# Optimization experiments

Hardware: AMD Instinct MI355X
Metric: run time of the kernel (lower is better)

## Reference

```python
import jax, jax.numpy as jnp
import numpy as np

N_NODES = 100_000
N_EDGES_RAND = 800_000
N_GRAPHS = 2048
IN_FEATS = 74        # CanonicalAtomFeaturizer size
HEADS = 4            # dgllife GAT default num_heads
OUT_FEATS = 32       # dgllife GAT default hidden_feats=[32,32]
PRED_DIM = 128
NEG_SLOPE = 0.2      # dgllife default alpha


def setup_inputs() -> dict:
    key = jax.random.key(0)
    ks = jax.random.split(key, 16)
    feats = jax.random.normal(ks[0], (N_NODES, IN_FEATS), jnp.float32)
    src_r = jax.random.randint(ks[1], (N_EDGES_RAND,), 0, N_NODES, dtype=jnp.int32)
    dst_r = jax.random.randint(ks[2], (N_EDGES_RAND,), 0, N_NODES, dtype=jnp.int32)
    loops = jnp.arange(N_NODES, dtype=jnp.int32)  # self-loops -> no zero in-degree
    src = jnp.concatenate([src_r, loops])
    dst = jnp.concatenate([dst_r, loops])
    # sorted, every graph non-empty, ~49 nodes per molecule
    graph_ids = ((jnp.arange(N_NODES, dtype=jnp.int64) * N_GRAPHS) // N_NODES).astype(jnp.int32)

    def lin(k, i, o):
        return (jax.random.normal(k, (i, o), jnp.float32) / np.sqrt(i)).astype(jnp.float32)

    HF = HEADS * OUT_FEATS
    return {
        'feats': feats, 'src': src, 'dst': dst, 'graph_ids': graph_ids,
        'fc1_w': lin(ks[3], IN_FEATS, HF),
        'attn_l1': jax.random.normal(ks[4], (HEADS, OUT_FEATS), jnp.float32) * 0.1,
        'attn_r1': jax.random.normal(ks[5], (HEADS, OUT_FEATS), jnp.float32) * 0.1,
        'res1_w': lin(ks[6], IN_FEATS, HF),   # residual proj (in != heads*out)
        'bias1': jnp.zeros((HF,), jnp.float32),
        'fc2_w': lin(ks[7], HF, HF),
        'attn_l2': jax.random.normal(ks[8], (HEADS, OUT_FEATS), jnp.float32) * 0.1,
        'attn_r2': jax.random.normal(ks[9], (HEADS, OUT_FEATS), jnp.float32) * 0.1,
        'bias2': jnp.zeros((HF,), jnp.float32),
        'ww': lin(ks[10], OUT_FEATS, 1),
        'wb': jnp.zeros((1,), jnp.float32),
        'tw': lin(ks[11], 2 * OUT_FEATS, PRED_DIM),
        'tb': jnp.zeros((PRED_DIM,), jnp.float32),
    }


def _gat_conv(h, src, dst, fc_w, attn_l, attn_r, bias, res):
    # h: (N, Din) -> (N, H, F). Faithful to dgl.nn.GATConv (bias=True, residual=True).
    N = h.shape[0]
    feat = (h @ fc_w).reshape(N, HEADS, OUT_FEATS)          # (N,H,F)
    el = jnp.sum(feat * attn_l, axis=-1)                    # (N,H)
    er = jnp.sum(feat * attn_r, axis=-1)                    # (N,H)
    e = jax.nn.leaky_relu(el[src] + er[dst], NEG_SLOPE)     # (E,H)
    # edge softmax over incoming edges of each dst node (numerically stable)
    emax = jax.ops.segment_max(e, dst, num_segments=N)      # (N,H)
    ee = jnp.exp(e - emax[dst])
    denom = jax.ops.segment_sum(ee, dst, num_segments=N)    # (N,H)
    a = ee / denom[dst]                                     # (E,H)
    rst = jax.ops.segment_sum(a[:, :, None] * feat[src], dst, num_segments=N)  # (N,H,F)
    return rst + res + bias.reshape(1, HEADS, OUT_FEATS)


def reference(feats, src, dst, graph_ids, fc1_w, attn_l1, attn_r1, res1_w, bias1,
              fc2_w, attn_l2, attn_r2, bias2, ww, wb, tw, tb):
    N = feats.shape[0]
    # Layer 1: residual needs projection (74 != 128); agg 'flatten' + ELU
    res1 = (feats @ res1_w).reshape(N, HEADS, OUT_FEATS)
    h1 = _gat_conv(feats, src, dst, fc1_w, attn_l1, attn_r1, bias1, res1)
    h1 = jax.nn.elu(h1.reshape(N, HEADS * OUT_FEATS))
    # Layer 2: identity residual (128 == heads*out); agg 'mean', no activation
    res2 = h1.reshape(N, HEADS, OUT_FEATS)
    h2 = _gat_conv(h1, src, dst, fc2_w, attn_l2, attn_r2, bias2, res2)
    node_feats = jnp.mean(h2, axis=1)                       # (N, 32)
    # WeightedSumAndMax readout
    w = jax.nn.sigmoid(node_feats @ ww + wb)                # (N,1)
    h_sum = jax.ops.segment_sum(w * node_feats, graph_ids, num_segments=N_GRAPHS)
    h_max = jax.ops.segment_max(node_feats, graph_ids, num_segments=N_GRAPHS)
    g = jnp.concatenate([h_sum, h_max], axis=-1)            # (B, 64)
    return g @ tw + tb                                      # (B, PRED_DIM)
```

## Files before the change

### kernel.cpp

```cpp
#include <hip/hip_runtime.h>
#include <hip/hip_bf16.h>


#define HEADS 4
#define OUTF 32
#define HF 128
#define IN_FEATS 74
#define PRED_DIM 128
#define NEG_SLOPE 0.2f
#define NEG_INF_ENC 0x007fffffu
#define LOG2E 1.4426950408889634f
#define KP1 48
#define KP2 64

typedef __hip_bfloat16 bf16;
typedef __hip_bfloat162 bf16x2;
typedef __attribute__((ext_vector_type(8))) short bf16x8v;
typedef __attribute__((ext_vector_type(4))) float f32x4v;
typedef __attribute__((ext_vector_type(2))) float f32x2v;

__device__ __forceinline__ unsigned enc_f(float f) {
  unsigned u = __float_as_uint(f);
  return (u & 0x80000000u) ? ~u : (u | 0x80000000u);
}
__device__ __forceinline__ float dec_f(unsigned k) {
  return (k & 0x80000000u) ? __uint_as_float(k & 0x7fffffffu)
                           : __uint_as_float(~k);
}
__device__ __forceinline__ unsigned pack_bf16(float a, float b) {
  bf16x2 h = __float22bfloat162_rn(make_float2(a, b));
  return *(unsigned*)&h;
}
__device__ __forceinline__ float2 unpack_bf16(unsigned u) {
  bf16x2 h = *(bf16x2*)&u;
  return __bfloat1622float2(h);
}
__device__ __forceinline__ float lrelu(float v) {
  return fmaxf(v, NEG_SLOPE * v);
}

__global__ __launch_bounds__(256) void hist_prep(
    const int* __restrict__ dst, int* __restrict__ deg,
    int* __restrict__ rank, float* __restrict__ hsum,
    unsigned* __restrict__ hmax, int E, int g32,
    const float* __restrict__ W1, const float* __restrict__ W2,
    const float* __restrict__ W3, unsigned* __restrict__ WT1,
    unsigned* __restrict__ WT2, unsigned* __restrict__ WT3) {
  int t = blockIdx.x * 256 + threadIdx.x;
  if (t < g32) {
    hsum[t] = 0.f;
    hmax[t] = NEG_INF_ENC;
  }
  if (t < 128 * KP1) {
    int c = t / KP1, kp = t % KP1;
    int k = kp * 2;
    float a1 = (k < IN_FEATS) ? W1[k * HF + c] : 0.f;
    float b1 = (k + 1 < IN_FEATS) ? W1[(k + 1) * HF + c] : 0.f;
    float a2 = (k < IN_FEATS) ? W2[k * HF + c] : 0.f;
    float b2 = (k + 1 < IN_FEATS) ? W2[(k + 1) * HF + c] : 0.f;
    WT1[t] = pack_bf16(a1, b1);
    WT2[t] = pack_bf16(a2, b2);
  } else if (t - 128 * KP1 < 128 * KP2) {
    int u = t - 128 * KP1;
    int c = u / KP2, kp = u % KP2;
    int k = kp * 2;
    WT3[u] = pack_bf16(W3[k * HF + c], W3[(k + 1) * HF + c]);
  }
  if (t < E) rank[t] = atomicAdd(&deg[dst[t]], 1);
}

__global__ __launch_bounds__(256) void scan12_kernel(
    const int* __restrict__ deg, int* __restrict__ row_ptr,
    int* __restrict__ bsum, int* __restrict__ bpre,
    int* __restrict__ ticket, int N, int E) {
  const int base = blockIdx.x * 2048;
  const int tbase = base + threadIdx.x * 8;
  int vals[8];
  int tsum = 0;
#pragma unroll
  for (int i = 0; i < 8; ++i) {
    int idx = tbase + i;
    vals[i] = (idx < N) ? deg[idx] : 0;
    tsum += vals[i];
  }
  const int lane = threadIdx.x & 63, wv = threadIdx.x >> 6;
  int incl = tsum;
#pragma unroll
  for (int off = 1; off < 64; off <<= 1) {
    int nv = __shfl_up(incl, off);
    if (lane >= off) incl += nv;
  }
  __shared__ int wsum[4];
  __shared__ int isLast;
  if (lane == 63) wsum[wv] = incl;
  __syncthreads();
  int woff = 0;
  for (int w = 0; w < wv; ++w) woff += wsum[w];
  int run = woff + incl - tsum;
#pragma unroll
  for (int i = 0; i < 8; ++i) {
    int idx = tbase + i;
    if (idx < N) row_ptr[idx] = run;
    run += vals[i];
  }
  if (threadIdx.x == 255) {
    bsum[blockIdx.x] = woff + incl;
    __threadfence();
    int t = atomicAdd(ticket, 1);
    isLast = (t == (int)gridDim.x - 1);
  }
  __syncthreads();
  if (isLast) {
    if (threadIdx.x < 64) {
      __threadfence();
      const int NB = gridDim.x;
      int running = 0;
      for (int c = 0; c < NB; c += 64) {
        int v = (c + lane < NB) ? bsum[c + lane] : 0;
        int incl2 = v;
#pragma unroll
        for (int off = 1; off < 64; off <<= 1) {
          int nv = __shfl_up(incl2, off);
          if (lane >= off) incl2 += nv;
        }
        if (c + lane < NB) bpre[c + lane] = running + incl2 - v;
        running += __shfl(incl2, 63);
      }
    }
    __syncthreads();
    if (threadIdx.x == 0) row_ptr[N] = E - bpre[N >> 11];
  }
}


template <int K>
__device__ __forceinline__ bf16x8v load_a_f32(const float* __restrict__ X,
                                              int row, int N, int ks, int q) {
  unsigned v[4] = {0u, 0u, 0u, 0u};
  if (row < N) {
    const float* base = X + (size_t)row * K;
    int k = ks * 32 + q * 8;
#pragma unroll
    for (int j = 0; j < 4; ++j) {
      int kk = k + j * 2;
      if (kk + 1 < K) {
        float2 f = *(const float2*)&base[kk];
        v[j] = pack_bf16(f.x, f.y);
      } else if (kk < K) {
        v[j] = pack_bf16(base[kk], 0.f);
      }
    }
  }
  union { unsigned u[4]; bf16x8v v8; } r;
  r.u[0] = v[0]; r.u[1] = v[1]; r.u[2] = v[2]; r.u[3] = v[3];
  return r.v8;
}

__device__ __forceinline__ void scores_epilogue(
    const f32x4v* acc, const float* __restrict__ attn_l,
    const float* __restrict__ attn_r, float* __restrict__ el,
    float* __restrict__ er, int n0, int w, int q, int cc, int N) {
#pragma unroll
  for (int r = 0; r < 4; ++r) {
    int n = n0 + w * 16 + q * 4 + r;
    float pls[4], prs[4];
#pragma unroll
    for (int h = 0; h < 4; ++h) {
      float pl = acc[2 * h][r] * attn_l[h * 32 + cc] +
                 acc[2 * h + 1][r] * attn_l[h * 32 + 16 + cc];
      float pr = acc[2 * h][r] * attn_r[h * 32 + cc] +
                 acc[2 * h + 1][r] * attn_r[h * 32 + 16 + cc];
#pragma unroll
      for (int off = 1; off < 16; off <<= 1) {
        pl += __shfl_xor(pl, off);
        pr += __shfl_xor(pr, off);
      }
      pls[h] = pl;
      prs[h] = pr;
    }
    if (cc == 0 && n < N) {
#pragma unroll
      for (int h = 0; h < 4; ++h) {
        el[n * HEADS + h] = pls[h] * LOG2E;
        er[n * HEADS + h] = prs[h] * LOG2E;
      }
    }
  }
}

template <int K, int KP>
__global__ __launch_bounds__(256) void mfma_gemm(
    const bf16* __restrict__ X, const unsigned* __restrict__ WT,
    const float* __restrict__ attn_l, const float* __restrict__ attn_r,
    bf16* __restrict__ out, float* __restrict__ el, float* __restrict__ er,
    int N) {
  const int tid = threadIdx.x;
  const int w = tid >> 6;
  const int lane = tid & 63;
  const int cc = lane & 15;
  const int q = lane >> 4;
  const int n0 = blockIdx.x * 64;
  const int arow = n0 + w * 16 + cc;

  f32x4v acc[8];
#pragma unroll
  for (int t = 0; t < 8; ++t) acc[t] = f32x4v{0.f, 0.f, 0.f, 0.f};

  constexpr int KSTEPS = (K + 31) / 32;
#pragma unroll
  for (int ks = 0; ks < KSTEPS; ++ks) {
    bf16x8v a = *(const bf16x8v*)&X[(size_t)arow * K + ks * 32 + q * 8];
#pragma unroll
    for (int t = 0; t < 8; ++t) {
      bf16x8v b = *(const bf16x8v*)&WT[(t * 16 + cc) * KP + ks * 16 + q * 4];
      acc[t] = __builtin_amdgcn_mfma_f32_16x16x32_bf16(a, b, acc[t], 0, 0, 0);
    }
  }
#pragma unroll
  for (int r = 0; r < 4; ++r) {
    int n = n0 + w * 16 + q * 4 + r;
    if (n < N) {
#pragma unroll
      for (int t = 0; t < 8; ++t)
        out[(size_t)n * HF + t * 16 + cc] = __float2bfloat16(acc[t][r]);
    }
  }
  scores_epilogue(acc, attn_l, attn_r, el, er, n0, w, q, cc, N);
}

__global__ __launch_bounds__(256) void scat_mfma1(
    const int* __restrict__ src, const int* __restrict__ dst,
    const int* __restrict__ row_ptr, const int* __restrict__ bpre,
    const int* __restrict__ rank, int* __restrict__ ssorted, int E, int SB,
    const float* __restrict__ X, const unsigned* __restrict__ WT1,
    const unsigned* __restrict__ WT2, const float* __restrict__ attn_l,
    const float* __restrict__ attn_r, bf16* __restrict__ outA,
    bf16* __restrict__ outB, float* __restrict__ el, float* __restrict__ er,
    int N) {
  if ((int)blockIdx.x < SB) {
    int e = blockIdx.x * 256 + threadIdx.x;
    if (e >= E) return;
    if (e < 16) ssorted[E + e] = 0;
    int d = dst[e];
    ssorted[row_ptr[d] + bpre[d >> 11] + rank[e]] = src[e];
    return;
  }
  const int tid = threadIdx.x;
  const int w = tid >> 6;
  const int lane = tid & 63;
  const int cc = lane & 15;
  const int q = lane >> 4;
  const int n0 = ((int)blockIdx.x - SB) * 64;
  const int arow = n0 + w * 16 + cc;

  f32x4v acc1[8], acc2[8];
#pragma unroll
  for (int t = 0; t < 8; ++t) {
    acc1[t] = f32x4v{0.f, 0.f, 0.f, 0.f};
    acc2[t] = f32x4v{0.f, 0.f, 0.f, 0.f};
  }

  constexpr int KSTEPS = (IN_FEATS + 31) / 32;
#pragma unroll
  for (int ks = 0; ks < KSTEPS; ++ks) {
    bf16x8v a = load_a_f32<IN_FEATS>(X, arow, N, ks, q);
#pragma unroll
    for (int t = 0; t < 8; ++t) {
      bf16x8v b1 = *(const bf16x8v*)&WT1[(t * 16 + cc) * KP1 + ks * 16 + q * 4];
      bf16x8v b2 = *(const bf16x8v*)&WT2[(t * 16 + cc) * KP1 + ks * 16 + q * 4];
      acc1[t] = __builtin_amdgcn_mfma_f32_16x16x32_bf16(a, b1, acc1[t], 0, 0, 0);
      acc2[t] = __builtin_amdgcn_mfma_f32_16x16x32_bf16(a, b2, acc2[t], 0, 0, 0);
    }
  }
#pragma unroll
  for (int r = 0; r < 4; ++r) {
    int n = n0 + w * 16 + q * 4 + r;
    if (n < N) {
#pragma unroll
      for (int t = 0; t < 8; ++t) {
        outA[(size_t)n * HF + t * 16 + cc] = __float2bfloat16(acc1[t][r]);
        outB[(size_t)n * HF + t * 16 + cc] = __float2bfloat16(acc2[t][r]);
      }
    }
  }
  scores_epilogue(acc1, attn_l, attn_r, el, er, n0, w, q, cc, N);
}


#define E8_LOAD(i, e_)                                                      \
  const int s##i = __builtin_amdgcn_readfirstlane(ssorted[e_]);             \
  const float xl##i = el[(unsigned)s##i * HEADS + h];                       \
  const unsigned fu##i = *(const unsigned*)&feat[(unsigned)s##i * HF + c2];
#define E8_CALC(i)                                                          \
  {                                                                         \
    float xx = __builtin_amdgcn_exp2f(lrelu(xl##i + ern));                  \
    f32x2v ff;                                                              \
    ff.x = __uint_as_float(fu##i << 16);                                    \
    ff.y = __uint_as_float(fu##i & 0xffff0000u);                            \
    ssum += xx;                                                             \
    axy = __builtin_elementwise_fma(f32x2v{xx, xx}, ff, axy);               \
  }
#define E8_CALC_PRED(i, e_)                                                 \
  {                                                                         \
    float xx = __builtin_amdgcn_exp2f(lrelu(xl##i + ern));                  \
    xx = ((e_) + i < re) ? xx : 0.f;                                        \
    f32x2v ff;                                                              \
    ff.x = __uint_as_float(fu##i << 16);                                    \
    ff.y = __uint_as_float(fu##i & 0xffff0000u);                            \
    ssum += xx;                                                             \
    axy = __builtin_elementwise_fma(f32x2v{xx, xx}, ff, axy);               \
  }

#define AGG_LOOP                                                            \
  f32x2v axy = {0.f, 0.f};                                                  \
  float ssum = 0.f;                                                         \
  const int dg = re - rb;                                                   \
  if (dg <= 8) {                                                            \
    E8_LOAD(0, rb) E8_LOAD(1, rb + 1) E8_LOAD(2, rb + 2)                    \
    E8_LOAD(3, rb + 3) E8_LOAD(4, rb + 4) E8_LOAD(5, rb + 5)                \
    E8_LOAD(6, rb + 6) E8_LOAD(7, rb + 7)                                   \
    E8_CALC_PRED(0, rb) E8_CALC_PRED(1, rb) E8_CALC_PRED(2, rb)             \
    E8_CALC_PRED(3, rb) E8_CALC_PRED(4, rb) E8_CALC_PRED(5, rb)             \
    E8_CALC_PRED(6, rb) E8_CALC_PRED(7, rb)                                 \
  } else if (dg <= 16) {                                                    \
    E8_LOAD(0, rb) E8_LOAD(1, rb + 1) E8_LOAD(2, rb + 2)                    \
    E8_LOAD(3, rb + 3) E8_LOAD(4, rb + 4) E8_LOAD(5, rb + 5)                \
    E8_LOAD(6, rb + 6) E8_LOAD(7, rb + 7)                                   \
    E8_LOAD(8, rb + 8) E8_LOAD(9, rb + 9) E8_LOAD(10, rb + 10)              \
    E8_LOAD(11, rb + 11) E8_LOAD(12, rb + 12) E8_LOAD(13, rb + 13)          \
    E8_LOAD(14, rb + 14) E8_LOAD(15, rb + 15)                               \
    E8_CALC(0) E8_CALC(1) E8_CALC(2) E8_CALC(3)                             \
    E8_CALC(4) E8_CALC(5) E8_CALC(6) E8_CALC(7)                             \
    E8_CALC_PRED(8, rb) E8_CALC_PRED(9, rb) E8_CALC_PRED(10, rb)            \
    E8_CALC_PRED(11, rb) E8_CALC_PRED(12, rb) E8_CALC_PRED(13, rb)          \
    E8_CALC_PRED(14, rb) E8_CALC_PRED(15, rb)                               \
  } else {                                                                  \
    int e = rb;                                                             \
    for (; e + 8 <= re; e += 8) {                                           \
      E8_LOAD(0, e) E8_LOAD(1, e + 1) E8_LOAD(2, e + 2) E8_LOAD(3, e + 3)   \
      E8_LOAD(4, e + 4) E8_LOAD(5, e + 5) E8_LOAD(6, e + 6)                 \
      E8_LOAD(7, e + 7)                                                     \
      E8_CALC(0) E8_CALC(1) E8_CALC(2) E8_CALC(3)                           \
      E8_CALC(4) E8_CALC(5) E8_CALC(6) E8_CALC(7)                           \
    }                                                                       \
    if (e < re) {                                                           \
      E8_LOAD(0, e) E8_LOAD(1, e + 1) E8_LOAD(2, e + 2) E8_LOAD(3, e + 3)   \
      E8_LOAD(4, e + 4) E8_LOAD(5, e + 5) E8_LOAD(6, e + 6)                 \
      E8_LOAD(7, e + 7)                                                     \
      E8_CALC_PRED(0, e) E8_CALC_PRED(1, e) E8_CALC_PRED(2, e)              \
      E8_CALC_PRED(3, e) E8_CALC_PRED(4, e) E8_CALC_PRED(5, e)              \
      E8_CALC_PRED(6, e) E8_CALC_PRED(7, e)                                 \
    }                                                                       \
  }                                                                         \
  float ax = axy.x, ay = axy.y;

__global__ __launch_bounds__(256) void agg1_fused(
    const int* __restrict__ row_ptr, const int* __restrict__ bpre,
    const int* __restrict__ ssorted, const float* __restrict__ el,
    const float* __restrict__ er, const bf16* __restrict__ feat,
    const bf16* __restrict__ res, bf16* __restrict__ H,
    const float* __restrict__ bias, int N) {
  int n = blockIdx.x * 4 + (threadIdx.x >> 6);
  if (n >= N) return;
  const int lane = threadIdx.x & 63;
  const int c2 = lane * 2, h = lane >> 4;
  const int rb =
      __builtin_amdgcn_readfirstlane(row_ptr[n] + bpre[n >> 11]);
  const int re =
      __builtin_amdgcn_readfirstlane(row_ptr[n + 1] + bpre[(n + 1) >> 11]);
  const float ern = er[(unsigned)n * HEADS + h];

  AGG_LOOP

  float inv = 1.f / ssum;
  float2 r = unpack_bf16(*(const unsigned*)&res[(unsigned)n * HF + c2]);
  float2 bi = *(const float2*)&bias[c2];
  float vx = fmaf(ax, inv, r.x + bi.x);
  float vy = fmaf(ay, inv, r.y + bi.y);
  vx = (vx > 0.f) ? vx : expm1f(vx);
  vy = (vy > 0.f) ? vy : expm1f(vy);
  *(unsigned*)&H[(unsigned)n * HF + c2] = pack_bf16(vx, vy);
}

__global__ __launch_bounds__(256) void agg2_fused(
    const int* __restrict__ row_ptr, const int* __restrict__ bpre,
    const int* __restrict__ ssorted, const float* __restrict__ el,
    const float* __restrict__ er, const bf16* __restrict__ feat,
    const bf16* __restrict__ h1, const float* __restrict__ bias,
    const float* __restrict__ ww, const float* __restrict__ wb,
    const int* __restrict__ gids, float* __restrict__ hsum,
    unsigned* __restrict__ hmax, int N) {
  int n = blockIdx.x * 4 + (threadIdx.x >> 6);
  if (n >= N) return;
  const int lane = threadIdx.x & 63;
  const int c2 = lane * 2, h = lane >> 4;
  const int rb =
      __builtin_amdgcn_readfirstlane(row_ptr[n] + bpre[n >> 11]);
  const int re =
      __builtin_amdgcn_readfirstlane(row_ptr[n + 1] + bpre[(n + 1) >> 11]);
  const float ern = er[(unsigned)n * HEADS + h];

  AGG_LOOP

  float inv = 1.f / ssum;
  float2 r = unpack_bf16(*(const unsigned*)&h1[(unsigned)n * HF + c2]);
  float2 bi = *(const float2*)&bias[c2];
  ax = fmaf(ax, inv, r.x + bi.x);
  ay = fmaf(ay, inv, r.y + bi.y);
#pragma unroll
  for (int off = 16; off < 64; off <<= 1) {
    ax += __shfl_xor(ax, off);
    ay += __shfl_xor(ay, off);
  }
  ax *= 0.25f;
  ay *= 0.25f;
  int c = c2 & 31;
  float d = fmaf(ax, ww[c], ay * ww[c + 1]);
#pragma unroll
  for (int off = 1; off < 16; off <<= 1) d += __shfl_xor(d, off);
  float wv = 1.f / (1.f + __expf(-(d + wb[0])));
  if (lane < 16) {
    int g = gids[n];
    atomicAdd(&hsum[g * OUTF + c], wv * ax);
    atomicAdd(&hsum[g * OUTF + c + 1], wv * ay);
    atomicMax(&hmax[g * OUTF + c], enc_f(ax));
    atomicMax(&hmax[g * OUTF + c + 1], enc_f(ay));
  }
}

__global__ __launch_bounds__(256) void final_gemm_kernel(
    const float* __restrict__ hsum, const unsigned* __restrict__ hmax,
    const float* __restrict__ tw, const float* __restrict__ tb,
    float* __restrict__ out, int G) {
  __shared__ float tws[64 * PRED_DIM];
  for (int i = threadIdx.x; i < 64 * PRED_DIM; i += 256) tws[i] = tw[i];
  __syncthreads();
  int g = blockIdx.x * 2 + (threadIdx.x >> 7);
  int p = threadIdx.x & 127;
  if (g >= G) return;
  float acc = tb[p];
#pragma unroll
  for (int k = 0; k < OUTF; ++k)
    acc = fmaf(hsum[g * OUTF + k], tws[k * PRED_DIM + p], acc);
#pragma unroll
  for (int k = 0; k < OUTF; ++k)
    acc = fmaf(dec_f(hmax[g * OUTF + k]), tws[(OUTF + k) * PRED_DIM + p], acc);
  out[(size_t)g * PRED_DIM + p] = acc;
}

static inline int cdiv(long long a, int b) { return (int)((a + b - 1) / b); }

extern "C" void kernel_launch(void* const* d_in, const int* in_sizes, int n_in,
                              void* d_out, int out_size, void* d_ws,
                              size_t ws_size, hipStream_t stream) {
  const float* feats   = (const float*)d_in[0];
  const int*   src     = (const int*)d_in[1];
  const int*   dst     = (const int*)d_in[2];
  const int*   gids    = (const int*)d_in[3];
  const float* fc1_w   = (const float*)d_in[4];
  const float* attn_l1 = (const float*)d_in[5];
  const float* attn_r1 = (const float*)d_in[6];
  const float* res1_w  = (const float*)d_in[7];
  const float* bias1   = (const float*)d_in[8];
  const float* fc2_w   = (const float*)d_in[9];
  const float* attn_l2 = (const float*)d_in[10];
  const float* attn_r2 = (const float*)d_in[11];
  const float* bias2   = (const float*)d_in[12];
  const float* ww      = (const float*)d_in[13];
  const float* wb      = (const float*)d_in[14];
  const float* tw      = (const float*)d_in[15];
  const float* tb      = (const float*)d_in[16];
  float* out = (float*)d_out;

  const int N = in_sizes[0] / IN_FEATS;
  const int E = in_sizes[1];
  const int G = out_size / PRED_DIM;
  const int NB = cdiv(N, 2048);

  bf16* A = (bf16*)d_ws;
  bf16* B = A + (size_t)N * HF;
  bf16* H = B + (size_t)N * HF;
  float* el = (float*)(H + (size_t)N * HF);
  float* er = el + (size_t)N * HEADS;
  float* hsum = er + (size_t)N * HEADS;
  unsigned* hmax = (unsigned*)(hsum + (size_t)G * OUTF);
  int* deg     = (int*)(hmax + (size_t)G * OUTF);
  int* ticket  = deg + N;
  int* row_ptr = deg + N + 1;
  int* ssorted = row_ptr + (N + 1);
  int* rank    = ssorted + E + 16;
  int* bsum    = rank + E;
  int* bpre    = bsum + NB;
  unsigned* WT1 = (unsigned*)(((uintptr_t)(bpre + NB) + 15) &
                              ~(uintptr_t)15);
  unsigned* WT2 = WT1 + 128 * KP1;
  unsigned* WT3 = WT2 + 128 * KP1;

  const int gblk = cdiv(N, 64);
  const int nwblk = cdiv(N, 4);
  const int SB = cdiv(E, 256);

  hipMemsetAsync(deg, 0, (size_t)(N + 1) * sizeof(int), stream);
  hist_prep<<<SB, 256, 0, stream>>>(dst, deg, rank, hsum, hmax, E, G * OUTF,
                                    fc1_w, res1_w, fc2_w, WT1, WT2, WT3);
  scan12_kernel<<<NB, 256, 0, stream>>>(deg, row_ptr, bsum, bpre, ticket, N,
                                        E);

  scat_mfma1<<<SB + gblk, 256, 0, stream>>>(
      src, dst, row_ptr, bpre, rank, ssorted, E, SB, feats, WT1, WT2,
      attn_l1, attn_r1, A, B, el, er, N);
  agg1_fused<<<nwblk, 256, 0, stream>>>(row_ptr, bpre, ssorted, el, er, A, B,
                                        H, bias1, N);

  mfma_gemm<HF, KP2><<<gblk, 256, 0, stream>>>(
      H, WT3, attn_l2, attn_r2, A, el, er, N);
  agg2_fused<<<nwblk, 256, 0, stream>>>(row_ptr, bpre, ssorted, el, er, A, H,
                                        bias2, ww, wb, gids, hsum, hmax, N);

  final_gemm_kernel<<<cdiv(G, 2), 256, 0, stream>>>(hsum, hmax, tw, tb, out, G);
}
```

Baseline: 345.9 us.

## Regroup kernels: fuse layer-1 GEMM with histogram, stage GEMM output via LDS

The deg memset moves into the weight-prep kernel, and the layer-1 dual GEMM now runs in the same launch as the degree histogram atomics, while the CSR scatter becomes its own kernel after the scan. GEMM output tiles are written to swizzled shared memory and then stored to global as 16-byte rows instead of scattered 2-byte stores. The aim is to overlap GEMM work with the atomic-heavy histogram, drop a memset call, and coalesce the bf16 output writes. In exchange it adds LDS use and an extra kernel launch for the scatter.

```diff
diff --git a/kernel.cpp b/kernel.cpp
--- a/kernel.cpp
+++ b/kernel.cpp
@@ -39,18 +39,13 @@
   return fmaxf(v, NEG_SLOPE * v);
 }
 
-__global__ __launch_bounds__(256) void hist_prep(
-    const int* __restrict__ dst, int* __restrict__ deg,
-    int* __restrict__ rank, float* __restrict__ hsum,
-    unsigned* __restrict__ hmax, int E, int g32,
+__global__ __launch_bounds__(256) void prep0(
     const float* __restrict__ W1, const float* __restrict__ W2,
     const float* __restrict__ W3, unsigned* __restrict__ WT1,
-    unsigned* __restrict__ WT2, unsigned* __restrict__ WT3) {
+    unsigned* __restrict__ WT2, unsigned* __restrict__ WT3,
+    int* __restrict__ deg, int N) {
   int t = blockIdx.x * 256 + threadIdx.x;
-  if (t < g32) {
-    hsum[t] = 0.f;
-    hmax[t] = NEG_INF_ENC;
-  }
+  if (t <= N) deg[t] = 0;
   if (t < 128 * KP1) {
     int c = t / KP1, kp = t % KP1;
     int k = kp * 2;
@@ -66,7 +61,6 @@
     int k = kp * 2;
     WT3[u] = pack_bf16(W3[k * HF + c], W3[(k + 1) * HF + c]);
   }
-  if (t < E) rank[t] = atomicAdd(&deg[dst[t]], 1);
 }
 
 __global__ __launch_bounds__(256) void scan12_kernel(
@@ -132,6 +126,17 @@
   }
 }
 
+__global__ __launch_bounds__(256) void scatter_kernel(
+    const int* __restrict__ src, const int* __restrict__ dst,
+    const int* __restrict__ row_ptr, const int* __restrict__ bpre,
+    const int* __restrict__ rank, int* __restrict__ ssorted, int E) {
+  int e = blockIdx.x * 256 + threadIdx.x;
+  if (e >= E) return;
+  if (e < 16) ssorted[E + e] = 0;
+  int d = dst[e];
+  ssorted[row_ptr[d] + bpre[d >> 11] + rank[e]] = src[e];
+}
+
 
 template <int K>
 __device__ __forceinline__ bf16x8v load_a_f32(const float* __restrict__ X,
@@ -188,12 +193,51 @@
   }
 }
 
-template <int K, int KP>
-__global__ __launch_bounds__(256) void mfma_gemm(
-    const bf16* __restrict__ X, const unsigned* __restrict__ WT,
-    const float* __restrict__ attn_l, const float* __restrict__ attn_r,
-    bf16* __restrict__ out, float* __restrict__ el, float* __restrict__ er,
-    int N) {
+__device__ __forceinline__ void store_tile(short* my, const f32x4v* acc,
+                                           bf16* __restrict__ out, int n0w,
+                                           int cc, int q, int lane, int N) {
+#pragma unroll
+  for (int t = 0; t < 8; ++t) {
+#pragma unroll
+    for (int r = 0; r < 4; ++r) {
+      int row = q * 4 + r;
+      int col = t * 16 + cc;
+      bf16 hv = __float2bfloat16(acc[t][r]);
+      my[row * 128 + (col ^ ((row & 7) << 3))] = *(short*)&hv;
+    }
+  }
+  int row = lane >> 2, qt = lane & 3;
+  int n = n0w + row;
+  if (n < N) {
+    int sw = (row & 7) << 3;
+    uint4* gp = (uint4*)&out[(size_t)n * HF + qt * 32];
+#pragma unroll
+    for (int j = 0; j < 4; ++j) {
+      int c0 = qt * 32 + j * 8;
+      gp[j] = *(const uint4*)&my[row * 128 + (c0 ^ sw)];
+    }
+  }
+}
+
+__global__ __launch_bounds__(256) void mfma1_hist(
+    const float* __restrict__ X, const unsigned* __restrict__ WT1,
+    const unsigned* __restrict__ WT2, const float* __restrict__ attn_l,
+    const float* __restrict__ attn_r, bf16* __restrict__ outA,
+    bf16* __restrict__ outB, float* __restrict__ el, float* __restrict__ er,
+    int N, int gblk,
+    const int* __restrict__ dst, int* __restrict__ deg,
+    int* __restrict__ rank, float* __restrict__ hsum,
+    unsigned* __restrict__ hmax, int E, int g32) {
+  __shared__ __align__(16) short cst[4][2048];
+  if ((int)blockIdx.x >= gblk) {
+    int e = ((int)blockIdx.x - gblk) * 256 + threadIdx.x;
+    if (e < g32) {
+      hsum[e] = 0.f;
+      hmax[e] = NEG_INF_ENC;
+    }
+    if (e < E) rank[e] = atomicAdd(&deg[dst[e]], 1);
+    return;
+  }
   const int tid = threadIdx.x;
   const int w = tid >> 6;
   const int lane = tid & 63;
@@ -202,88 +246,61 @@
   const int n0 = blockIdx.x * 64;
   const int arow = n0 + w * 16 + cc;
 
-  f32x4v acc[8];
-#pragma unroll
-  for (int t = 0; t < 8; ++t) acc[t] = f32x4v{0.f, 0.f, 0.f, 0.f};
-
-  constexpr int KSTEPS = (K + 31) / 32;
+  f32x4v acc1[8], acc2[8];
+#pragma unroll
+  for (int t = 0; t < 8; ++t) {
+    acc1[t] = f32x4v{0.f, 0.f, 0.f, 0.f};
+    acc2[t] = f32x4v{0.f, 0.f, 0.f, 0.f};
+  }
+
+  constexpr int KSTEPS = (IN_FEATS + 31) / 32;
 #pragma unroll
   for (int ks = 0; ks < KSTEPS; ++ks) {
-    bf16x8v a = *(const bf16x8v*)&X[(size_t)arow * K + ks * 32 + q * 8];
+    bf16x8v a = load_a_f32<IN_FEATS>(X, arow, N, ks, q);
 #pragma unroll
     for (int t = 0; t < 8; ++t) {
-      bf16x8v b = *(const bf16x8v*)&WT[(t * 16 + cc) * KP + ks * 16 + q * 4];
-      acc[t] = __builtin_amdgcn_mfma_f32_16x16x32_bf16(a, b, acc[t], 0, 0, 0);
-    }
-  }
-#pragma unroll
-  for (int r = 0; r < 4; ++r) {
-    int n = n0 + w * 16 + q * 4 + r;
-    if (n < N) {
-#pragma unroll
-      for (int t = 0; t < 8; ++t)
-        out[(size_t)n * HF + t * 16 + cc] = __float2bfloat16(acc[t][r]);
-    }
-  }
-  scores_epilogue(acc, attn_l, attn_r, el, er, n0, w, q, cc, N);
-}
-
-__global__ __launch_bounds__(256) void scat_mfma1(
-    const int* __restrict__ src, const int* __restrict__ dst,
-    const int* __restrict__ row_ptr, const int* __restrict__ bpre,
-    const int* __restrict__ rank, int* __restrict__ ssorted, int E, int SB,
-    const float* __restrict__ X, const unsigned* __restrict__ WT1,
-    const unsigned* __restrict__ WT2, const float* __restrict__ attn_l,
-    const float* __restrict__ attn_r, bf16* __restrict__ outA,
-    bf16* __restrict__ outB, float* __restrict__ el, float* __restrict__ er,
+      bf16x8v b1 = *(const bf16x8v*)&WT1[(t * 16 + cc) * KP1 + ks * 16 + q * 4];
+      bf16x8v b2 = *(const bf16x8v*)&WT2[(t * 16 + cc) * KP1 + ks * 16 + q * 4];
+      acc1[t] = __builtin_amdgcn_mfma_f32_16x16x32_bf16(a, b1, acc1[t], 0, 0, 0);
+      acc2[t] = __builtin_amdgcn_mfma_f32_16x16x32_bf16(a, b2, acc2[t], 0, 0, 0);
+    }
+  }
+  store_tile(&cst[w][0], acc1, outA, n0 + w * 16, cc, q, lane, N);
+  store_tile(&cst[w][0], acc2, outB, n0 + w * 16, cc, q, lane, N);
+  scores_epilogue(acc1, attn_l, attn_r, el, er, n0, w, q, cc, N);
+}
+
+template <int K, int KP>
+__global__ __launch_bounds__(256) void mfma_gemm(
+    const bf16* __restrict__ X, const unsigned* __restrict__ WT,
+    const float* __restrict__ attn_l, const float* __restrict__ attn_r,
+    bf16* __restrict__ out, float* __restrict__ el, float* __restrict__ er,
     int N) {
-  if ((int)blockIdx.x < SB) {
-    int e = blockIdx.x * 256 + threadIdx.x;
-    if (e >= E) return;
-    if (e < 16) ssorted[E + e] = 0;
-    int d = dst[e];
-    ssorted[row_ptr[d] + bpre[d >> 11] + rank[e]] = src[e];
-    return;
-  }
+  __shared__ __align__(16) short cst[4][2048];
   const int tid = threadIdx.x;
   const int w = tid >> 6;
   const int lane = tid & 63;
   const int cc = lane & 15;
   const int q = lane >> 4;
-  const int n0 = ((int)blockIdx.x - SB) * 64;
+  const int n0 = blockIdx.x * 64;
   const int arow = n0 + w * 16 + cc;
 
-  f32x4v acc1[8], acc2[8];
-#pragma unroll
-  for (int t = 0; t < 8; ++t) {
-    acc1[t] = f32x4v{0.f, 0.f, 0.f, 0.f};
-    acc2[t] = f32x4v{0.f, 0.f, 0.f, 0.f};
-  }
-
-  constexpr int KSTEPS = (IN_FEATS + 31) / 32;
+  f32x4v acc[8];
+#pragma unroll
+  for (int t = 0; t < 8; ++t) acc[t] = f32x4v{0.f, 0.f, 0.f, 0.f};
+
+  constexpr int KSTEPS = (K + 31) / 32;
 #pragma unroll
   for (int ks = 0; ks < KSTEPS; ++ks) {
-    bf16x8v a = load_a_f32<IN_FEATS>(X, arow, N, ks, q);
+    bf16x8v a = *(const bf16x8v*)&X[(size_t)arow * K + ks * 32 + q * 8];
 #pragma unroll
     for (int t = 0; t < 8; ++t) {
-      bf16x8v b1 = *(const bf16x8v*)&WT1[(t * 16 + cc) * KP1 + ks * 16 + q * 4];
-      bf16x8v b2 = *(const bf16x8v*)&WT2[(t * 16 + cc) * KP1 + ks * 16 + q * 4];
-      acc1[t] = __builtin_amdgcn_mfma_f32_16x16x32_bf16(a, b1, acc1[t], 0, 0, 0);
-      acc2[t] = __builtin_amdgcn_mfma_f32_16x16x32_bf16(a, b2, acc2[t], 0, 0, 0);
-    }
-  }
-#pragma unroll
-  for (int r = 0; r < 4; ++r) {
-    int n = n0 + w * 16 + q * 4 + r;
-    if (n < N) {
-#pragma unroll
-      for (int t = 0; t < 8; ++t) {
-        outA[(size_t)n * HF + t * 16 + cc] = __float2bfloat16(acc1[t][r]);
-        outB[(size_t)n * HF + t * 16 + cc] = __float2bfloat16(acc2[t][r]);
-      }
-    }
-  }
-  scores_epilogue(acc1, attn_l, attn_r, el, er, n0, w, q, cc, N);
+      bf16x8v b = *(const bf16x8v*)&WT[(t * 16 + cc) * KP + ks * 16 + q * 4];
+      acc[t] = __builtin_amdgcn_mfma_f32_16x16x32_bf16(a, b, acc[t], 0, 0, 0);
+    }
+  }
+  store_tile(&cst[w][0], acc, out, n0 + w * 16, cc, q, lane, N);
+  scores_epilogue(acc, attn_l, attn_r, el, er, n0, w, q, cc, N);
 }
 
 
@@ -500,15 +517,16 @@
   const int nwblk = cdiv(N, 4);
   const int SB = cdiv(E, 256);
 
-  hipMemsetAsync(deg, 0, (size_t)(N + 1) * sizeof(int), stream);
-  hist_prep<<<SB, 256, 0, stream>>>(dst, deg, rank, hsum, hmax, E, G * OUTF,
-                                    fc1_w, res1_w, fc2_w, WT1, WT2, WT3);
+  prep0<<<cdiv(N + 1, 256), 256, 0, stream>>>(fc1_w, res1_w, fc2_w, WT1, WT2,
+                                              WT3, deg, N);
+  mfma1_hist<<<gblk + SB, 256, 0, stream>>>(
+      feats, WT1, WT2, attn_l1, attn_r1, A, B, el, er, N, gblk,
+      dst, deg, rank, hsum, hmax, E, G * OUTF);
   scan12_kernel<<<NB, 256, 0, stream>>>(deg, row_ptr, bsum, bpre, ticket, N,
                                         E);
-
-  scat_mfma1<<<SB + gblk, 256, 0, stream>>>(
-      src, dst, row_ptr, bpre, rank, ssorted, E, SB, feats, WT1, WT2,
-      attn_l1, attn_r1, A, B, el, er, N);
+  scatter_kernel<<<SB, 256, 0, stream>>>(src, dst, row_ptr, bpre, rank,
+                                         ssorted, E);
+
   agg1_fused<<<nwblk, 256, 0, stream>>>(row_ptr, bpre, ssorted, el, er, A, B,
                                         H, bias1, N);
 
```

Result: no change. 349.2 us (+1.0%).
